# Optimization experiments

Measured on AMD Instinct MI355X. Metric: run time of the kernel, lower is better.

The kernel has to match this reference:

```python
import jax, jax.numpy as jnp
import numpy as np

NUM, D_MODEL, D_INNER, D_STATE, D_CONV, DT_RANK = 8, 512, 1024, 16, 4, 32


def silu(v):
    return v * jax.nn.sigmoid(v)


def setup_inputs() -> dict:
    key = jax.random.key(0)
    ks = jax.random.split(key, 8)
    B, L = 4, 1024

    def nrm(k, shape, fan_in):
        return jax.random.normal(k, shape, jnp.float32) / np.float32(np.sqrt(fan_in))

    x = jax.random.normal(ks[0], (B, L, D_MODEL), jnp.float32)
    in_proj_w = nrm(ks[1], (NUM, 2 * D_INNER, D_MODEL), D_MODEL)
    conv_w = nrm(ks[2], (NUM, D_INNER, D_CONV), D_CONV)
    conv_b = jnp.zeros((NUM, D_INNER), jnp.float32)
    x_proj_w = nrm(ks[3], (NUM, DT_RANK + 2 * D_STATE, D_INNER), D_INNER)
    dt_proj_w = nrm(ks[4], (NUM, D_INNER, DT_RANK), DT_RANK)
    dt_proj_b = jnp.full((NUM, D_INNER), -4.6, jnp.float32)  # softplus -> ~0.01 dt
    # S4D-real init: A_log = log(1..d_state), broadcast over channels/layers
    A_log = jnp.broadcast_to(
        jnp.log(jnp.arange(1, D_STATE + 1, dtype=jnp.float32)), (NUM, D_INNER, D_STATE)
    ).copy()
    Dskip = jnp.ones((NUM, D_INNER), jnp.float32)
    out_proj_w = nrm(ks[5], (NUM, D_MODEL, D_INNER), D_INNER)
    return dict(x=x, in_proj_w=in_proj_w, conv_w=conv_w, conv_b=conv_b,
                x_proj_w=x_proj_w, dt_proj_w=dt_proj_w, dt_proj_b=dt_proj_b,
                A_log=A_log, Dskip=Dskip, out_proj_w=out_proj_w)


def mamba_layer(x, Wi, cw, cb, Wx, Wdt, bdt, A_log, Dsk, Wo):
    Bsz, L, _ = x.shape
    # in_proj -> (B, L, 2*d_inner), split into x branch and gate z
    xz = jnp.einsum('bld,ed->ble', x, Wi)
    xin, z = jnp.split(xz, 2, axis=-1)
    # causal depthwise conv over time, then SiLU
    u = xin.transpose(0, 2, 1)  # (B, d_inner, L)
    u = jax.lax.conv_general_dilated(
        u, cw[:, None, :], (1,), [(D_CONV - 1, 0)],
        dimension_numbers=('NCH', 'OIH', 'NCH'), feature_group_count=D_INNER)
    u = silu(u + cb[None, :, None])
    u = u.transpose(0, 2, 1)  # (B, L, d_inner)
    # input-dependent dt, B, C
    dbc = jnp.einsum('bld,ed->ble', u, Wx)  # (B, L, dt_rank + 2*d_state)
    dt = dbc[..., :DT_RANK]
    Bm = dbc[..., DT_RANK:DT_RANK + D_STATE]
    Cm = dbc[..., DT_RANK + D_STATE:]
    delta = jax.nn.softplus(jnp.einsum('blr,dr->bld', dt, Wdt) + bdt)  # (B, L, d_inner)
    A = -jnp.exp(A_log)  # (d_inner, d_state)

    def step(h, inp):
        d_t, B_t, C_t, u_t = inp  # (B,d_inner), (B,s), (B,s), (B,d_inner)
        dA = jnp.exp(d_t[..., None] * A)  # (B, d_inner, s)
        h = dA * h + (d_t * u_t)[..., None] * B_t[:, None, :]
        y = jnp.einsum('bds,bs->bd', h, C_t)
        return h, y

    h0 = jnp.zeros((Bsz, D_INNER, D_STATE), x.dtype)
    xs = (delta.transpose(1, 0, 2), Bm.transpose(1, 0, 2),
          Cm.transpose(1, 0, 2), u.transpose(1, 0, 2))
    _, ys = jax.lax.scan(step, h0, xs)  # ys: (L, B, d_inner)
    y = ys.transpose(1, 0, 2) + u * Dsk
    y = y * silu(z)
    return jnp.einsum('bld,ed->ble', y, Wo)


def reference(x, in_proj_w, conv_w, conv_b, x_proj_w, dt_proj_w, dt_proj_b, A_log, Dskip, out_proj_w):
    for i in range(NUM):
        x = mamba_layer(x, in_proj_w[i], conv_w[i], conv_b[i], x_proj_w[i],
                        dt_proj_w[i], dt_proj_b[i], A_log[i], Dskip[i], out_proj_w[i])
    return x
```

## Files before the change

kernel.cpp:

```cpp
#include <hip/hip_runtime.h>
#include <math.h>

#define B_SZ   4
#define LSEQ   1024
#define DMODEL 512
#define DINNER 1024
#define DSTATE 16
#define DCONV  4
#define DTRANK 32
#define NLAYER 8
#define NROWS  (B_SZ*LSEQ)
#define CHUNK  32
#define NCHUNK (LSEQ/CHUNK)
#define KPAD   40

__device__ __forceinline__ float sigmoid_(float x){ return 1.f/(1.f+__expf(-x)); }
__device__ __forceinline__ float softplus_(float v){
    return fmaxf(v,0.f) + __logf(1.f + __expf(-fabsf(v)));
}

typedef __attribute__((ext_vector_type(8))) short bf16x8;
typedef __attribute__((ext_vector_type(4))) short shortx4;
typedef __attribute__((ext_vector_type(4))) float f32x4;

__device__ __forceinline__ short f2bf(float f){
    unsigned int u = __float_as_uint(f);
    u = (u + 0x7FFFu + ((u >> 16) & 1u)) >> 16;
    return (short)u;
}
__device__ __forceinline__ float bf2f(short s){
    unsigned int u = ((unsigned int)(unsigned short)s) << 16;
    return __uint_as_float(u);
}

__global__ __launch_bounds__(256) void split_k(
    const float* __restrict__ in, short* __restrict__ hi, short* __restrict__ lo)
{
    long i = ((long)blockIdx.x*256 + threadIdx.x)*4;
    float4 x = *reinterpret_cast<const float4*>(&in[i]);
    shortx4 h, l;
    h.x=f2bf(x.x); l.x=f2bf(x.x-bf2f(h.x));
    h.y=f2bf(x.y); l.y=f2bf(x.y-bf2f(h.y));
    h.z=f2bf(x.z); l.z=f2bf(x.z-bf2f(h.z));
    h.w=f2bf(x.w); l.w=f2bf(x.w-bf2f(h.w));
    *reinterpret_cast<shortx4*>(&hi[i]) = h;
    *reinterpret_cast<shortx4*>(&lo[i]) = l;
}

__global__ __launch_bounds__(256) void split_w3(
    const float* __restrict__ wi, const float* __restrict__ wo,
    const float* __restrict__ wx,
    short* __restrict__ wih, short* __restrict__ wil,
    short* __restrict__ woh, short* __restrict__ wol,
    short* __restrict__ wxh, short* __restrict__ wxl)
{
    long bx = blockIdx.x;
    const float* src; short *ph, *pl; long base;
    if      (bx < 1024) { src = wi; ph = wih; pl = wil; base = bx*1024; }
    else if (bx < 1536) { src = wo; ph = woh; pl = wol; base = (bx-1024)*1024; }
    else                { src = wx; ph = wxh; pl = wxl; base = (bx-1536)*1024; }
    long i = base + (long)threadIdx.x*4;
    float4 x = *reinterpret_cast<const float4*>(&src[i]);
    shortx4 h, l;
    h.x=f2bf(x.x); l.x=f2bf(x.x-bf2f(h.x));
    h.y=f2bf(x.y); l.y=f2bf(x.y-bf2f(h.y));
    h.z=f2bf(x.z); l.z=f2bf(x.z-bf2f(h.z));
    h.w=f2bf(x.w); l.w=f2bf(x.w-bf2f(h.w));
    *reinterpret_cast<shortx4*>(&ph[i]) = h;
    *reinterpret_cast<shortx4*>(&pl[i]) = l;
}

template<int BM,int BN,int EPI,bool SPLITK>
__global__ __launch_bounds__(256,4) void gemm_bs_nt(
    const short* __restrict__ Agh, const short* __restrict__ Agl, int lda,
    const short* __restrict__ Bgh, const short* __restrict__ Bgl, int ldb,
    float* __restrict__ C, int ldc,
    short* __restrict__ Ch, short* __restrict__ Cl, int K, int ksl)
{
    constexpr int MREP = BM/32;
    constexpr int NREP = BN/32;
    constexpr int ACH  = BM/64;
    constexpr int BCH  = BN/64;
    __shared__ __align__(16) short Ahs[BM*KPAD], Als[BM*KPAD];
    __shared__ __align__(16) short Bhs[BN*KPAD], Bls[BN*KPAD];

    const int tid  = threadIdx.x;
    const int lane = tid & 63;
    const int wave = tid >> 6;
    const int wm = wave >> 1, wn = wave & 1;
    const int m0 = blockIdx.y * BM, n0 = blockIdx.x * BN;
    const int fr = lane & 15, fg = lane >> 4;
    const int k0 = SPLITK ? blockIdx.z * ksl : 0;

    int ar[ACH], ak[ACH];
#pragma unroll
    for (int j=0;j<ACH;j++){ int c = tid + j*256; ar[j]=c>>2; ak[j]=(c&3)*8; }
    int br[BCH], bk[BCH];
#pragma unroll
    for (int j=0;j<BCH;j++){ int c = tid + j*256; br[j]=c>>2; bk[j]=(c&3)*8; }

    f32x4 acc[MREP][NREP];
#pragma unroll
    for (int m=0;m<MREP;m++)
#pragma unroll
        for (int n=0;n<NREP;n++) acc[m][n] = (f32x4)0.f;

    bf16x8 rah[ACH], ral[ACH], rbh[BCH], rbl[BCH];

    auto load_tile = [&](int kt){
#pragma unroll
        for (int j=0;j<ACH;j++){
            long o = (long)(m0+ar[j])*lda + kt + ak[j];
            rah[j] = *reinterpret_cast<const bf16x8*>(&Agh[o]);
            ral[j] = *reinterpret_cast<const bf16x8*>(&Agl[o]);
        }
#pragma unroll
        for (int j=0;j<BCH;j++){
            long o = (long)(n0+br[j])*ldb + kt + bk[j];
            rbh[j] = *reinterpret_cast<const bf16x8*>(&Bgh[o]);
            rbl[j] = *reinterpret_cast<const bf16x8*>(&Bgl[o]);
        }
    };

    load_tile(k0);
    const int NK = (SPLITK ? ksl : K) >> 5;
    for (int s=0; s<NK; ++s){
#pragma unroll
        for (int j=0;j<ACH;j++){
            *reinterpret_cast<bf16x8*>(&Ahs[ar[j]*KPAD + ak[j]]) = rah[j];
            *reinterpret_cast<bf16x8*>(&Als[ar[j]*KPAD + ak[j]]) = ral[j];
        }
#pragma unroll
        for (int j=0;j<BCH;j++){
            *reinterpret_cast<bf16x8*>(&Bhs[br[j]*KPAD + bk[j]]) = rbh[j];
            *reinterpret_cast<bf16x8*>(&Bls[br[j]*KPAD + bk[j]]) = rbl[j];
        }
        __syncthreads();
        if (s+1 < NK) load_tile(k0 + ((s+1) << 5));

        bf16x8 bh[NREP], bl[NREP];
#pragma unroll
        for (int n=0;n<NREP;n++){
            int row = wn*(BN/2) + n*16 + fr;
            bh[n] = *reinterpret_cast<const bf16x8*>(&Bhs[row*KPAD + fg*8]);
            bl[n] = *reinterpret_cast<const bf16x8*>(&Bls[row*KPAD + fg*8]);
        }
#pragma unroll
        for (int m=0;m<MREP;m++){
            int row = wm*(BM/2) + m*16 + fr;
            bf16x8 ah = *reinterpret_cast<const bf16x8*>(&Ahs[row*KPAD + fg*8]);
            bf16x8 al = *reinterpret_cast<const bf16x8*>(&Als[row*KPAD + fg*8]);
#pragma unroll
            for (int n=0;n<NREP;n++){
                acc[m][n] = __builtin_amdgcn_mfma_f32_16x16x32_bf16(al, bh[n], acc[m][n],0,0,0);
                acc[m][n] = __builtin_amdgcn_mfma_f32_16x16x32_bf16(ah, bl[n], acc[m][n],0,0,0);
                acc[m][n] = __builtin_amdgcn_mfma_f32_16x16x32_bf16(ah, bh[n], acc[m][n],0,0,0);
            }
        }
        __syncthreads();
    }

#pragma unroll
    for (int m=0;m<MREP;m++)
#pragma unroll
      for (int n=0;n<NREP;n++)
#pragma unroll
        for (int q=0;q<4;q++){
            int row = m0 + wm*(BM/2) + m*16 + fg*4 + q;
            int col = n0 + wn*(BN/2) + n*16 + fr;
            float v = acc[m][n][q];
            if (EPI==0) {
                C[(long)row*ldc + col] = v;
            } else if (EPI==1) {
                short h = f2bf(v);
                Ch[(long)row*ldc + col] = h;
                Cl[(long)row*ldc + col] = f2bf(v - bf2f(h));
            } else {
                C[((long)blockIdx.z*NROWS + row)*ldc + col] = v;
            }
        }
}

__global__ __launch_bounds__(256) void reduce_dbc(
    const float* __restrict__ part, float* __restrict__ dbc)
{
    long i = ((long)blockIdx.x*256 + threadIdx.x)*4;
    float4 a = *reinterpret_cast<const float4*>(&part[i]);
#pragma unroll
    for (int s=1;s<8;s++){
        float4 b = *reinterpret_cast<const float4*>(&part[(long)s*(NROWS*64) + i]);
        a.x+=b.x; a.y+=b.y; a.z+=b.z; a.w+=b.w;
    }
    *reinterpret_cast<float4*>(&dbc[i]) = a;
}

__global__ __launch_bounds__(256) void conv_silu_k(
    const float* __restrict__ xz, const float* __restrict__ cw,
    const float* __restrict__ cb, float* __restrict__ u,
    short* __restrict__ uh, short* __restrict__ ul)
{
    int idx = blockIdx.x*256 + threadIdx.x;
    int d4  = idx & (DINNER/4 - 1);
    int row = idx >> 8;
    int t   = row & (LSEQ-1);

    float4 cbv = *reinterpret_cast<const float4*>(&cb[d4*4]);
    float acc[4] = {cbv.x, cbv.y, cbv.z, cbv.w};
    float4 cw0 = *reinterpret_cast<const float4*>(&cw[d4*16 + 0]);
    float4 cw1 = *reinterpret_cast<const float4*>(&cw[d4*16 + 4]);
    float4 cw2 = *reinterpret_cast<const float4*>(&cw[d4*16 + 8]);
    float4 cw3 = *reinterpret_cast<const float4*>(&cw[d4*16 +12]);
    const float* pw[4] = {&cw0.x, &cw1.x, &cw2.x, &cw3.x};

#pragma unroll
    for (int j=0;j<DCONV;j++){
        int tt = t - (DCONV-1) + j;
        if (tt < 0) continue;
        float4 xv = *reinterpret_cast<const float4*>(&xz[(long)(row-(DCONV-1)+j)*2*DINNER + d4*4]);
        acc[0] = fmaf(xv.x, pw[0][j], acc[0]);
        acc[1] = fmaf(xv.y, pw[1][j], acc[1]);
        acc[2] = fmaf(xv.z, pw[2][j], acc[2]);
        acc[3] = fmaf(xv.w, pw[3][j], acc[3]);
    }
    float4 o;
    o.x = acc[0]*sigmoid_(acc[0]);
    o.y = acc[1]*sigmoid_(acc[1]);
    o.z = acc[2]*sigmoid_(acc[2]);
    o.w = acc[3]*sigmoid_(acc[3]);
    long base = (long)row*DINNER + d4*4;
    *reinterpret_cast<float4*>(&u[base]) = o;
    shortx4 h, l;
    h.x=f2bf(o.x); l.x=f2bf(o.x-bf2f(h.x));
    h.y=f2bf(o.y); l.y=f2bf(o.y-bf2f(h.y));
    h.z=f2bf(o.z); l.z=f2bf(o.z-bf2f(h.z));
    h.w=f2bf(o.w); l.w=f2bf(o.w-bf2f(h.w));
    *reinterpret_cast<shortx4*>(&uh[base]) = h;
    *reinterpret_cast<shortx4*>(&ul[base]) = l;
}

#define DTP 36

__global__ __launch_bounds__(256) void scan_phaseA(
    const float* __restrict__ u, const float* __restrict__ dbc,
    const float* __restrict__ Alog, const float* __restrict__ Wdt,
    const float* __restrict__ bdt,
    float* __restrict__ hst, float* __restrict__ sd)
{
    __shared__ float Bsh[CHUNK*DSTATE];
    __shared__ float Dtsh[CHUNK*DTP];
    int bx = blockIdx.x;
    int dblk = bx & 3;
    int c    = (bx>>2) & (NCHUNK-1);
    int b    = bx >> 7;
    int d    = dblk*256 + threadIdx.x;

    {
        int i = threadIdx.x;
        int tr = i >> 3, c4 = (i & 7)*4;
        float4 dv = *reinterpret_cast<const float4*>(&dbc[(long)(b*LSEQ + c*CHUNK + tr)*64 + c4]);
        *reinterpret_cast<float4*>(&Dtsh[tr*DTP + c4]) = dv;
        for (int j = i; j < CHUNK*DSTATE; j += 256) {
            int r = j >> 4, s = j & 15;
            Bsh[j] = dbc[(long)(b*LSEQ + c*CHUNK + r)*64 + DTRANK + s];
        }
    }
    __syncthreads();

    float wdt[DTRANK];
#pragma unroll
    for (int q=0;q<DTRANK;q+=4)
        *reinterpret_cast<float4*>(&wdt[q]) = *reinterpret_cast<const float4*>(&Wdt[(long)d*DTRANK + q]);
    float bias = bdt[d];

    float As[DSTATE];
#pragma unroll
    for (int s=0;s<DSTATE;s++) As[s] = -__expf(Alog[d*DSTATE+s]);
    float h[DSTATE];
#pragma unroll
    for (int s=0;s<DSTATE;s++) h[s]=0.f;
    float sumd = 0.f;

    long baseU = (long)(b*LSEQ + c*CHUNK)*DINNER + d;
    for (int tt=0; tt<CHUNK; ++tt) {
        float v = bias;
#pragma unroll
        for (int r=0;r<DTRANK;r++) v = fmaf(Dtsh[tt*DTP + r], wdt[r], v);
        float dt = softplus_(v);
        float ut = u[baseU + (long)tt*DINNER];
        sumd += dt;
        float du = dt*ut;
#pragma unroll
        for (int s=0;s<DSTATE;s++)
            h[s] = fmaf(__expf(As[s]*dt), h[s], du*Bsh[tt*DSTATE+s]);
    }
    long ho = ((long)((b*NCHUNK + c)*DINNER) + d)*DSTATE;
#pragma unroll
    for (int s=0;s<DSTATE;s+=4)
        *reinterpret_cast<float4*>(&hst[ho+s]) = make_float4(h[s],h[s+1],h[s+2],h[s+3]);
    sd[(b*NCHUNK+c)*DINNER + d] = sumd;
}

__global__ __launch_bounds__(256) void scan_phaseB(
    const float* __restrict__ Alog, const float* __restrict__ sd,
    float* __restrict__ hst)
{
    int flat = blockIdx.x*256 + threadIdx.x;
    int s = flat & 15;
    int d = (flat >> 4) & (DINNER-1);
    int b = flat >> 14;
    float As = -__expf(Alog[d*DSTATE+s]);
    float H = 0.f;
    for (int c=0; c<NCHUNK; ++c) {
        long o = ((long)((b*NCHUNK+c)*DINNER)+d)*DSTATE + s;
        float hl  = hst[o];
        float sdc = sd[(b*NCHUNK+c)*DINNER + d];
        hst[o] = H;
        H = fmaf(__expf(As*sdc), H, hl);
    }
}

__global__ __launch_bounds__(256) void scan_phaseC(
    const float* __restrict__ xz, const float* __restrict__ u,
    const float* __restrict__ dbc, const float* __restrict__ Alog,
    const float* __restrict__ Wdt, const float* __restrict__ bdt,
    const float* __restrict__ hst, const float* __restrict__ Dsk,
    short* __restrict__ yh, short* __restrict__ yl)
{
    __shared__ float Bsh[CHUNK*DSTATE];
    __shared__ float Csh[CHUNK*DSTATE];
    __shared__ float Dtsh[CHUNK*DTP];
    int bx = blockIdx.x;
    int dblk = bx & 3;
    int c    = (bx>>2) & (NCHUNK-1);
    int b    = bx >> 7;
    int d    = dblk*256 + threadIdx.x;

    {
        int i = threadIdx.x;
        int tr = i >> 3, c4 = (i & 7)*4;
        float4 dv = *reinterpret_cast<const float4*>(&dbc[(long)(b*LSEQ + c*CHUNK + tr)*64 + c4]);
        *reinterpret_cast<float4*>(&Dtsh[tr*DTP + c4]) = dv;
        for (int j = i; j < CHUNK*DSTATE; j += 256) {
            int r = j >> 4, s = j & 15;
            long ro = (long)(b*LSEQ + c*CHUNK + r)*64;
            Bsh[j] = dbc[ro + DTRANK + s];
            Csh[j] = dbc[ro + DTRANK + DSTATE + s];
        }
    }
    __syncthreads();

    float wdt[DTRANK];
#pragma unroll
    for (int q=0;q<DTRANK;q+=4)
        *reinterpret_cast<float4*>(&wdt[q]) = *reinterpret_cast<const float4*>(&Wdt[(long)d*DTRANK + q]);
    float bias = bdt[d];

    float As[DSTATE];
#pragma unroll
    for (int s=0;s<DSTATE;s++) As[s] = -__expf(Alog[d*DSTATE+s]);
    float h[DSTATE];
    long ho = ((long)((b*NCHUNK + c)*DINNER) + d)*DSTATE;
#pragma unroll
    for (int s=0;s<DSTATE;s+=4){
        float4 hv = *reinterpret_cast<const float4*>(&hst[ho+s]);
        h[s]=hv.x; h[s+1]=hv.y; h[s+2]=hv.z; h[s+3]=hv.w;
    }
    float Dd = Dsk[d];

    long baseU = (long)(b*LSEQ + c*CHUNK)*DINNER + d;
    long baseZ = (long)(b*LSEQ + c*CHUNK)*2*DINNER + DINNER + d;
    for (int tt=0; tt<CHUNK; ++tt) {
        float v = bias;
#pragma unroll
        for (int r=0;r<DTRANK;r++) v = fmaf(Dtsh[tt*DTP + r], wdt[r], v);
        float dt = softplus_(v);
        float ut = u[baseU + (long)tt*DINNER];
        float du = dt*ut;
        float y = 0.f;
#pragma unroll
        for (int s=0;s<DSTATE;s++){
            h[s] = fmaf(__expf(As[s]*dt), h[s], du*Bsh[tt*DSTATE+s]);
            y = fmaf(h[s], Csh[tt*DSTATE+s], y);
        }
        y = fmaf(ut, Dd, y);
        float zv = xz[baseZ + (long)tt*2*DINNER];
        y *= zv * sigmoid_(zv);
        short hh = f2bf(y);
        yh[baseU + (long)tt*DINNER] = hh;
        yl[baseU + (long)tt*DINNER] = f2bf(y - bf2f(hh));
    }
}

extern "C" void kernel_launch(void* const* d_in, const int* in_sizes, int n_in,
                              void* d_out, int out_size, void* d_ws, size_t ws_size,
                              hipStream_t stream)
{
    const float* x_in = (const float*)d_in[0];
    const float* Wi   = (const float*)d_in[1];
    const float* cw   = (const float*)d_in[2];
    const float* cb   = (const float*)d_in[3];
    const float* Wx   = (const float*)d_in[4];
    const float* Wdt  = (const float*)d_in[5];
    const float* bdt  = (const float*)d_in[6];
    const float* Alog = (const float*)d_in[7];
    const float* Dsk  = (const float*)d_in[8];
    const float* Wo   = (const float*)d_in[9];
    float* out = (float*)d_out;

    float* ws   = (float*)d_ws;
    float* xz   = ws;
    float* u    = xz  + 8388608;
    float* dbc  = u   + 4194304;
    float* hst  = dbc + 262144;
    float* sd   = hst + 2097152;
    short* sp   = (short*)(sd + 131072);
    short* srch = sp;
    short* srcl = srch + 2097152;
    short* wih  = srcl + 2097152;
    short* wil  = wih  + 1048576;
    short* woh  = wil  + 1048576;
    short* wol  = woh  + 524288;
    short* wxh  = wol  + 524288;
    short* wxl  = wxh  + 65536;
    short* yh   = wxl  + 65536;
    short* yl   = yh   + 4194304;

    split_k<<<NROWS*DMODEL/1024, 256, 0, stream>>>(x_in, srch, srcl);

    for (int l=0; l<NLAYER; ++l) {
        const float* Wi_l  = Wi  + (long)l*2*DINNER*DMODEL;
        const float* cw_l  = cw  + (long)l*DINNER*DCONV;
        const float* cb_l  = cb  + (long)l*DINNER;
        const float* Wx_l  = Wx  + (long)l*(DTRANK+2*DSTATE)*DINNER;
        const float* Wdt_l = Wdt + (long)l*DINNER*DTRANK;
        const float* bdt_l = bdt + (long)l*DINNER;
        const float* Al_l  = Alog+ (long)l*DINNER*DSTATE;
        const float* Dsk_l = Dsk + (long)l*DINNER;
        const float* Wo_l  = Wo  + (long)l*DMODEL*DINNER;

        split_w3<<<1600, 256, 0, stream>>>(Wi_l, Wo_l, Wx_l, wih, wil, woh, wol, wxh, wxl);

        gemm_bs_nt<128,64,0,false><<<dim3(2*DINNER/64, NROWS/128), 256, 0, stream>>>(
            srch, srcl, DMODEL, wih, wil, DMODEL, xz, 2*DINNER, nullptr, nullptr, DMODEL, DMODEL);

        conv_silu_k<<<NROWS*(DINNER/4)/256, 256, 0, stream>>>(xz, cw_l, cb_l, u, yh, yl);

        gemm_bs_nt<128,64,2,true><<<dim3(1, NROWS/128, 8), 256, 0, stream>>>(
            yh, yl, DINNER, wxh, wxl, DINNER, hst, 64, nullptr, nullptr, DINNER, DINNER/8);
        reduce_dbc<<<NROWS*64/1024, 256, 0, stream>>>(hst, dbc);

        scan_phaseA<<<B_SZ*NCHUNK*(DINNER/256), 256, 0, stream>>>(
            u, dbc, Al_l, Wdt_l, bdt_l, hst, sd);
        scan_phaseB<<<B_SZ*DINNER*DSTATE/256, 256, 0, stream>>>(Al_l, sd, hst);
        scan_phaseC<<<B_SZ*NCHUNK*(DINNER/256), 256, 0, stream>>>(
            xz, u, dbc, Al_l, Wdt_l, bdt_l, hst, Dsk_l, yh, yl);

        if (l == NLAYER-1) {
            gemm_bs_nt<64,64,0,false><<<dim3(DMODEL/64, NROWS/64), 256, 0, stream>>>(
                yh, yl, DINNER, woh, wol, DINNER, out, DMODEL, nullptr, nullptr, DINNER, DINNER);
        } else {
            gemm_bs_nt<64,64,1,false><<<dim3(DMODEL/64, NROWS/64), 256, 0, stream>>>(
                yh, yl, DINNER, woh, wol, DINNER, nullptr, DMODEL, srch, srcl, DINNER, DINNER);
        }
    }
}
```

Before: 1.332 ms.

## Batch weight splitting, drop fp32 u buffer, widen in_proj GEMM tile

All layers' weights are now split into bf16 hi/lo pairs by one upfront launch, replacing a split kernel per layer. The fp32 u buffer is removed: the scans rebuild u from its bf16 hi/lo pair, and scan_phaseC overwrites that pair in place with y. The in_proj GEMM moves to 128x128 tiles with a lower occupancy bound. Together these cut global memory traffic and launch count, at the cost of a larger weight workspace and more register pressure in the wider GEMM.

Result: no change. 1.326 ms (-0.5%).

```diff
diff --git a/kernel.cpp b/kernel.cpp
--- a/kernel.cpp
+++ b/kernel.cpp
@@ -13,6 +13,7 @@
 #define CHUNK  32
 #define NCHUNK (LSEQ/CHUNK)
 #define KPAD   40
+#define WSTRIDE 3276800L
 
 __device__ __forceinline__ float sigmoid_(float x){ return 1.f/(1.f+__expf(-x)); }
 __device__ __forceinline__ float softplus_(float v){
@@ -47,31 +48,30 @@
     *reinterpret_cast<shortx4*>(&lo[i]) = l;
 }
 
-__global__ __launch_bounds__(256) void split_w3(
+__global__ __launch_bounds__(256) void split_w_all(
     const float* __restrict__ wi, const float* __restrict__ wo,
-    const float* __restrict__ wx,
-    short* __restrict__ wih, short* __restrict__ wil,
-    short* __restrict__ woh, short* __restrict__ wol,
-    short* __restrict__ wxh, short* __restrict__ wxl)
-{
-    long bx = blockIdx.x;
+    const float* __restrict__ wx, short* __restrict__ wsp)
+{
+    int bx = blockIdx.x;
+    int l  = bx / 1600, r = bx % 1600;
+    short* lw = wsp + (long)l*WSTRIDE;
     const float* src; short *ph, *pl; long base;
-    if      (bx < 1024) { src = wi; ph = wih; pl = wil; base = bx*1024; }
-    else if (bx < 1536) { src = wo; ph = woh; pl = wol; base = (bx-1024)*1024; }
-    else                { src = wx; ph = wxh; pl = wxl; base = (bx-1536)*1024; }
+    if      (r < 1024) { src = wi + (long)l*1048576; base = (long)r*1024;        ph = lw;         pl = lw+1048576; }
+    else if (r < 1536) { src = wo + (long)l*524288;  base = (long)(r-1024)*1024; ph = lw+2097152; pl = lw+2621440; }
+    else               { src = wx + (long)l*65536;   base = (long)(r-1536)*1024; ph = lw+3145728; pl = lw+3211264; }
     long i = base + (long)threadIdx.x*4;
     float4 x = *reinterpret_cast<const float4*>(&src[i]);
-    shortx4 h, l;
-    h.x=f2bf(x.x); l.x=f2bf(x.x-bf2f(h.x));
-    h.y=f2bf(x.y); l.y=f2bf(x.y-bf2f(h.y));
-    h.z=f2bf(x.z); l.z=f2bf(x.z-bf2f(h.z));
-    h.w=f2bf(x.w); l.w=f2bf(x.w-bf2f(h.w));
+    shortx4 h, l4;
+    h.x=f2bf(x.x); l4.x=f2bf(x.x-bf2f(h.x));
+    h.y=f2bf(x.y); l4.y=f2bf(x.y-bf2f(h.y));
+    h.z=f2bf(x.z); l4.z=f2bf(x.z-bf2f(h.z));
+    h.w=f2bf(x.w); l4.w=f2bf(x.w-bf2f(h.w));
     *reinterpret_cast<shortx4*>(&ph[i]) = h;
-    *reinterpret_cast<shortx4*>(&pl[i]) = l;
-}
-
-template<int BM,int BN,int EPI,bool SPLITK>
-__global__ __launch_bounds__(256,4) void gemm_bs_nt(
+    *reinterpret_cast<shortx4*>(&pl[i]) = l4;
+}
+
+template<int BM,int BN,int EPI,bool SPLITK,int MINW>
+__global__ __launch_bounds__(256,MINW) void gemm_bs_nt(
     const short* __restrict__ Agh, const short* __restrict__ Agl, int lda,
     const short* __restrict__ Bgh, const short* __restrict__ Bgl, int ldb,
     float* __restrict__ C, int ldc,
@@ -196,7 +196,7 @@
 
 __global__ __launch_bounds__(256) void conv_silu_k(
     const float* __restrict__ xz, const float* __restrict__ cw,
-    const float* __restrict__ cb, float* __restrict__ u,
+    const float* __restrict__ cb,
     short* __restrict__ uh, short* __restrict__ ul)
 {
     int idx = blockIdx.x*256 + threadIdx.x;
@@ -222,18 +222,17 @@
         acc[2] = fmaf(xv.z, pw[2][j], acc[2]);
         acc[3] = fmaf(xv.w, pw[3][j], acc[3]);
     }
-    float4 o;
-    o.x = acc[0]*sigmoid_(acc[0]);
-    o.y = acc[1]*sigmoid_(acc[1]);
-    o.z = acc[2]*sigmoid_(acc[2]);
-    o.w = acc[3]*sigmoid_(acc[3]);
+    float o[4];
+    o[0] = acc[0]*sigmoid_(acc[0]);
+    o[1] = acc[1]*sigmoid_(acc[1]);
+    o[2] = acc[2]*sigmoid_(acc[2]);
+    o[3] = acc[3]*sigmoid_(acc[3]);
     long base = (long)row*DINNER + d4*4;
-    *reinterpret_cast<float4*>(&u[base]) = o;
     shortx4 h, l;
-    h.x=f2bf(o.x); l.x=f2bf(o.x-bf2f(h.x));
-    h.y=f2bf(o.y); l.y=f2bf(o.y-bf2f(h.y));
-    h.z=f2bf(o.z); l.z=f2bf(o.z-bf2f(h.z));
-    h.w=f2bf(o.w); l.w=f2bf(o.w-bf2f(h.w));
+    h.x=f2bf(o[0]); l.x=f2bf(o[0]-bf2f(h.x));
+    h.y=f2bf(o[1]); l.y=f2bf(o[1]-bf2f(h.y));
+    h.z=f2bf(o[2]); l.z=f2bf(o[2]-bf2f(h.z));
+    h.w=f2bf(o[3]); l.w=f2bf(o[3]-bf2f(h.w));
     *reinterpret_cast<shortx4*>(&uh[base]) = h;
     *reinterpret_cast<shortx4*>(&ul[base]) = l;
 }
@@ -241,7 +240,8 @@
 #define DTP 36
 
 __global__ __launch_bounds__(256) void scan_phaseA(
-    const float* __restrict__ u, const float* __restrict__ dbc,
+    const short* __restrict__ uh, const short* __restrict__ ul,
+    const float* __restrict__ dbc,
     const float* __restrict__ Alog, const float* __restrict__ Wdt,
     const float* __restrict__ bdt,
     float* __restrict__ hst, float* __restrict__ sd)
@@ -286,7 +286,8 @@
 #pragma unroll
         for (int r=0;r<DTRANK;r++) v = fmaf(Dtsh[tt*DTP + r], wdt[r], v);
         float dt = softplus_(v);
-        float ut = u[baseU + (long)tt*DINNER];
+        long ui = baseU + (long)tt*DINNER;
+        float ut = bf2f(uh[ui]) + bf2f(ul[ui]);
         sumd += dt;
         float du = dt*ut;
 #pragma unroll
@@ -320,11 +321,11 @@
 }
 
 __global__ __launch_bounds__(256) void scan_phaseC(
-    const float* __restrict__ xz, const float* __restrict__ u,
+    const float* __restrict__ xz,
+    short* uyh, short* uyl,
     const float* __restrict__ dbc, const float* __restrict__ Alog,
     const float* __restrict__ Wdt, const float* __restrict__ bdt,
-    const float* __restrict__ hst, const float* __restrict__ Dsk,
-    short* __restrict__ yh, short* __restrict__ yl)
+    const float* __restrict__ hst, const float* __restrict__ Dsk)
 {
     __shared__ float Bsh[CHUNK*DSTATE];
     __shared__ float Csh[CHUNK*DSTATE];
@@ -374,7 +375,8 @@
 #pragma unroll
         for (int r=0;r<DTRANK;r++) v = fmaf(Dtsh[tt*DTP + r], wdt[r], v);
         float dt = softplus_(v);
-        float ut = u[baseU + (long)tt*DINNER];
+        long ui = baseU + (long)tt*DINNER;
+        float ut = bf2f(uyh[ui]) + bf2f(uyl[ui]);
         float du = dt*ut;
         float y = 0.f;
 #pragma unroll
@@ -386,8 +388,8 @@
         float zv = xz[baseZ + (long)tt*2*DINNER];
         y *= zv * sigmoid_(zv);
         short hh = f2bf(y);
-        yh[baseU + (long)tt*DINNER] = hh;
-        yl[baseU + (long)tt*DINNER] = f2bf(y - bf2f(hh));
+        uyh[ui] = hh;
+        uyl[ui] = f2bf(y - bf2f(hh));
     }
 }
 
@@ -409,57 +411,51 @@
 
     float* ws   = (float*)d_ws;
     float* xz   = ws;
-    float* u    = xz  + 8388608;
-    float* dbc  = u   + 4194304;
+    float* dbc  = xz  + 8388608;
     float* hst  = dbc + 262144;
     float* sd   = hst + 2097152;
     short* sp   = (short*)(sd + 131072);
     short* srch = sp;
     short* srcl = srch + 2097152;
-    short* wih  = srcl + 2097152;
-    short* wil  = wih  + 1048576;
-    short* woh  = wil  + 1048576;
-    short* wol  = woh  + 524288;
-    short* wxh  = wol  + 524288;
-    short* wxl  = wxh  + 65536;
-    short* yh   = wxl  + 65536;
+    short* wsp  = srcl + 2097152;
+    short* yh   = wsp  + NLAYER*WSTRIDE;
     short* yl   = yh   + 4194304;
 
     split_k<<<NROWS*DMODEL/1024, 256, 0, stream>>>(x_in, srch, srcl);
+    split_w_all<<<NLAYER*1600, 256, 0, stream>>>(Wi, Wo, Wx, wsp);
 
     for (int l=0; l<NLAYER; ++l) {
-        const float* Wi_l  = Wi  + (long)l*2*DINNER*DMODEL;
         const float* cw_l  = cw  + (long)l*DINNER*DCONV;
         const float* cb_l  = cb  + (long)l*DINNER;
-        const float* Wx_l  = Wx  + (long)l*(DTRANK+2*DSTATE)*DINNER;
         const float* Wdt_l = Wdt + (long)l*DINNER*DTRANK;
         const float* bdt_l = bdt + (long)l*DINNER;
         const float* Al_l  = Alog+ (long)l*DINNER*DSTATE;
         const float* Dsk_l = Dsk + (long)l*DINNER;
-        const float* Wo_l  = Wo  + (long)l*DMODEL*DINNER;
-
-        split_w3<<<1600, 256, 0, stream>>>(Wi_l, Wo_l, Wx_l, wih, wil, woh, wol, wxh, wxl);
-
-        gemm_bs_nt<128,64,0,false><<<dim3(2*DINNER/64, NROWS/128), 256, 0, stream>>>(
+        short* lw  = wsp + (long)l*WSTRIDE;
+        short* wih = lw,            *wil = lw+1048576;
+        short* woh = lw+2097152,    *wol = lw+2621440;
+        short* wxh = lw+3145728,    *wxl = lw+3211264;
+
+        gemm_bs_nt<128,128,0,false,2><<<dim3(2*DINNER/128, NROWS/128), 256, 0, stream>>>(
             srch, srcl, DMODEL, wih, wil, DMODEL, xz, 2*DINNER, nullptr, nullptr, DMODEL, DMODEL);
 
-        conv_silu_k<<<NROWS*(DINNER/4)/256, 256, 0, stream>>>(xz, cw_l, cb_l, u, yh, yl);
-
-        gemm_bs_nt<128,64,2,true><<<dim3(1, NROWS/128, 8), 256, 0, stream>>>(
+        conv_silu_k<<<NROWS*(DINNER/4)/256, 256, 0, stream>>>(xz, cw_l, cb_l, yh, yl);
+
+        gemm_bs_nt<128,64,2,true,4><<<dim3(1, NROWS/128, 8), 256, 0, stream>>>(
             yh, yl, DINNER, wxh, wxl, DINNER, hst, 64, nullptr, nullptr, DINNER, DINNER/8);
         reduce_dbc<<<NROWS*64/1024, 256, 0, stream>>>(hst, dbc);
 
         scan_phaseA<<<B_SZ*NCHUNK*(DINNER/256), 256, 0, stream>>>(
-            u, dbc, Al_l, Wdt_l, bdt_l, hst, sd);
+            yh, yl, dbc, Al_l, Wdt_l, bdt_l, hst, sd);
         scan_phaseB<<<B_SZ*DINNER*DSTATE/256, 256, 0, stream>>>(Al_l, sd, hst);
         scan_phaseC<<<B_SZ*NCHUNK*(DINNER/256), 256, 0, stream>>>(
-            xz, u, dbc, Al_l, Wdt_l, bdt_l, hst, Dsk_l, yh, yl);
+            xz, yh, yl, dbc, Al_l, Wdt_l, bdt_l, hst, Dsk_l);
 
         if (l == NLAYER-1) {
-            gemm_bs_nt<64,64,0,false><<<dim3(DMODEL/64, NROWS/64), 256, 0, stream>>>(
+            gemm_bs_nt<64,64,0,false,4><<<dim3(DMODEL/64, NROWS/64), 256, 0, stream>>>(
                 yh, yl, DINNER, woh, wol, DINNER, out, DMODEL, nullptr, nullptr, DINNER, DINNER);
         } else {
-            gemm_bs_nt<64,64,1,false><<<dim3(DMODEL/64, NROWS/64), 256, 0, stream>>>(
+            gemm_bs_nt<64,64,1,false,4><<<dim3(DMODEL/64, NROWS/64), 256, 0, stream>>>(
                 yh, yl, DINNER, woh, wol, DINNER, nullptr, DMODEL, srch, srcl, DINNER, DINNER);
         }
     }
```
